# Performance work log

Measured on AMD Instinct MI355X. Metric: run time of the kernel, lower is better.

## Reference

```python
import jax, jax.numpy as jnp
import numpy as np

BUCKET_SIZE = 256
LOOK_BACKWARD = 1
LOOK_FORWARD = 0  # causal


def look_around(x, backward, forward, pad_value):
    # x: (b, n_buckets, w, ...) -> (b, n_buckets, w*(backward+forward+1), ...)
    n = x.shape[1]
    pads = [(0, 0)] * x.ndim
    pads[1] = (backward, forward)
    p = jnp.pad(x, pads, constant_values=pad_value)
    return jnp.concatenate([p[:, i:i + n] for i in range(backward + forward + 1)], axis=2)


def setup_inputs() -> dict:
    key = jax.random.key(0)
    kq, kk, kv = jax.random.split(key, 3)
    shape = (2, 16, 4096, 64)  # [batch, heads, seq, head_dim]
    q = jax.random.normal(kq, shape, dtype=jnp.float32)
    k = jax.random.normal(kk, shape, dtype=jnp.float32)
    v = jax.random.normal(kv, shape, dtype=jnp.float32)
    return {"q": q, "k": k, "v": v}


def reference(q, k, v):
    shape = q.shape
    t, e = shape[-2], shape[-1]
    merge = lambda x: x.reshape(-1, t, e)
    q, k, v = merge(q), merge(k), merge(v)
    b = q.shape[0]
    buckets = t // BUCKET_SIZE

    bucket_fn = lambda x: x.reshape(b, buckets, BUCKET_SIZE, e)
    bq, bk, bv = bucket_fn(q), bucket_fn(k), bucket_fn(v)

    bk = look_around(bk, LOOK_BACKWARD, LOOK_FORWARD, 0.0)
    bv = look_around(bv, LOOK_BACKWARD, LOOK_FORWARD, 0.0)

    ticker = jnp.arange(t, dtype=jnp.int32).reshape(1, buckets, BUCKET_SIZE)
    bq_t = ticker  # (1, buckets, w)
    bq_k = look_around(ticker, LOOK_BACKWARD, LOOK_FORWARD, -1)  # (1, buckets, w*(lb+lf+1))

    dots = jnp.einsum('bnie,bnje->bnij', bq, bk) * (e ** -0.5)
    mask_value = -jnp.finfo(dots.dtype).max

    causal_mask = bq_t[:, :, :, None] < bq_k[:, :, None, :]
    pad_mask = (bq_k == -1)[:, :, None, :]
    dots = jnp.where(causal_mask | pad_mask, mask_value, dots)

    attn = jax.nn.softmax(dots, axis=-1)
    out = jnp.einsum('bnij,bnje->bnie', attn, bv)
    return out.reshape(shape)
```

## Files before the change

### kernel.cpp

```cpp
#include <hip/hip_runtime.h>

typedef __bf16 bf16x8 __attribute__((ext_vector_type(8)));
typedef float f32x16 __attribute__((ext_vector_type(16)));
typedef int i32x2 __attribute__((ext_vector_type(2)));
typedef unsigned int u32;

#define NCH 8

static __device__ __forceinline__ u32 cvt_pk_bf16(float lo, float hi) {
    u32 r;
    asm("v_cvt_pk_bf16_f32 %0, %1, %2" : "=v"(r) : "v"(lo), "v"(hi));
    return r;
}

__global__ __launch_bounds__(512, 4)
void local_attn_kernel(const float* __restrict__ qg, const float* __restrict__ kg,
                       const float* __restrict__ vg, float* __restrict__ og)
{
    __shared__ __align__(16) __bf16 sK[2][64][64];
    __shared__ __align__(16) u32 sVp[2][64][32];

    const int bid = ((blockIdx.x & 7) << 6) | (blockIdx.x >> 3);
    const int bh = bid >> 4, bi = bid & 15;
    const int tid = threadIdx.x, w = tid >> 6;
    const int lane = tid & 63, l31 = lane & 31, h = lane >> 5;

    const long long base = (long long)bh << 18;
    const float* qp = qg + base + ((long long)bi << 14);
    const float* kp = kg + base + (((long long)(bi - 1)) << 14);
    const float* vp = vg + base + (((long long)(bi - 1)) << 14);
    float*       op = og + base + ((long long)bi << 14);

    bf16x8 qf[4];
    {
        const float QS = 0.18033688011112042f;
        const float* qrow = qp + (w * 32 + l31) * 64 + 8 * h;
#pragma unroll
        for (int ks = 0; ks < 4; ++ks) {
            float4 f0 = *(const float4*)(qrow + ks * 16);
            float4 f1 = *(const float4*)(qrow + ks * 16 + 4);
            bf16x8 t;
            t[0] = (__bf16)(f0.x * QS); t[1] = (__bf16)(f0.y * QS);
            t[2] = (__bf16)(f0.z * QS); t[3] = (__bf16)(f0.w * QS);
            t[4] = (__bf16)(f1.x * QS); t[5] = (__bf16)(f1.y * QS);
            t[6] = (__bf16)(f1.z * QS); t[7] = (__bf16)(f1.w * QS);
            qf[ks] = t;
        }
    }

    f32x16 o0, o1;
#pragma unroll
    for (int i = 0; i < 16; ++i) { o0[i] = 0.f; o1[i] = 0.f; }
    float lsum = 0.f;

    const int skey = tid >> 3, stg = tid & 7;
    const int kslot = (stg ^ (skey & 7)) << 3;
    const int vkp = tid >> 4, vd0 = (tid & 15) * 4;
    const int vkq = vkp >> 2, vj = vkp & 3;
    const float* kA = kp + skey * 64 + stg * 8;
    const float* vA = vp + (2 * vkp) * 64 + vd0;

    const int c0 = (bi == 0) ? 4 : 0;
    const int qpos = w * 32 + l31;
    const int wlim = 32 * w + 287;

    int cur = 0;
    float4 k0r, k1r, v0r, v1r;

#define STAGE_LOAD(c) do {                                   \
        const float* ks_ = kA + (c) * (64 * 64);             \
        k0r = *(const float4*)ks_;                           \
        k1r = *(const float4*)(ks_ + 4);                     \
        const float* vs_ = vA + (c) * (64 * 64);             \
        v0r = *(const float4*)vs_;                           \
        v1r = *(const float4*)(vs_ + 64);                    \
    } while (0)

#define STAGE_WRITE(buf) do {                                                     \
        union { u32 u[4]; bf16x8 b; } kv_;                                        \
        kv_.u[0] = cvt_pk_bf16(k0r.x, k0r.y);                                     \
        kv_.u[1] = cvt_pk_bf16(k0r.z, k0r.w);                                     \
        kv_.u[2] = cvt_pk_bf16(k1r.x, k1r.y);                                     \
        kv_.u[3] = cvt_pk_bf16(k1r.z, k1r.w);                                     \
        *(bf16x8*)&sK[buf][skey][kslot] = kv_.b;                                  \
        {                                                                         \
            const int r0 = vd0,     s0 = vkq ^ (r0 & 7) ^ ((r0 >> 2) & 7);        \
            const int r1 = vd0 + 1, s1 = vkq ^ (r1 & 7) ^ ((r1 >> 2) & 7);        \
            const int r2 = vd0 + 2, s2 = vkq ^ (r2 & 7) ^ ((r2 >> 2) & 7);        \
            const int r3 = vd0 + 3, s3 = vkq ^ (r3 & 7) ^ ((r3 >> 2) & 7);        \
            sVp[buf][r0][(s0 << 2) + vj] = cvt_pk_bf16(v0r.x, v1r.x);             \
            sVp[buf][r1][(s1 << 2) + vj] = cvt_pk_bf16(v0r.y, v1r.y);             \
            sVp[buf][r2][(s2 << 2) + vj] = cvt_pk_bf16(v0r.z, v1r.z);             \
            sVp[buf][r3][(s3 << 2) + vj] = cvt_pk_bf16(v0r.w, v1r.w);             \
        }                                                                         \
    } while (0)

    STAGE_LOAD(c0);
    STAGE_WRITE(0);

    for (int c = c0; c < NCH; ++c) {
        __syncthreads();
        const bool pf = (c + 1 < NCH);
        if (pf) STAGE_LOAD(c + 1);

        const int kbase = c * 64;
#pragma unroll
        for (int kt = 0; kt < 2; ++kt) {
            const int kb0 = kbase + 32 * kt;
            if (kb0 > wlim) continue;

            const int key = kt * 32 + l31;
            const int ksw = key & 7;
            bf16x8 kfa[4];
#pragma unroll
            for (int ks = 0; ks < 4; ++ks)
                kfa[ks] = *(const bf16x8*)&sK[cur][key][((ks * 2 + h) ^ ksw) << 3];
            f32x16 s;
#pragma unroll
            for (int i = 0; i < 16; ++i) s[i] = 0.f;
#pragma unroll
            for (int ks = 0; ks < 4; ++ks)
                s = __builtin_amdgcn_mfma_f32_32x32x16_bf16(kfa[ks], qf[ks], s, 0, 0, 0);

            float pv[16];
            const int jb = kb0 + 4 * h;
            if (kb0 + 31 <= 32 * w + 256) {
#pragma unroll
                for (int r = 0; r < 16; ++r) {
                    pv[r] = __builtin_amdgcn_exp2f(s[r]);
                    lsum += pv[r];
                }
            } else {
#pragma unroll
                for (int r = 0; r < 16; ++r) {
                    const int j = jb + (r & 3) + 8 * (r >> 2);
                    float e = __builtin_amdgcn_exp2f(s[r]);
                    pv[r] = (j > qpos + 256) ? 0.f : e;
                    lsum += pv[r];
                }
            }

            u32 wds[8];
#pragma unroll
            for (int m = 0; m < 8; ++m)
                wds[m] = cvt_pk_bf16(pv[2 * m], pv[2 * m + 1]);

#pragma unroll
            for (int kis = 0; kis < 2; ++kis) {
                i32x2 r02 = __builtin_amdgcn_permlane32_swap(
                    (int)wds[4 * kis + 0], (int)wds[4 * kis + 2], false, false);
                i32x2 r13 = __builtin_amdgcn_permlane32_swap(
                    (int)wds[4 * kis + 1], (int)wds[4 * kis + 3], false, false);
                union { u32 u[4]; bf16x8 b; } pu;
                pu.u[0] = (u32)r02.x; pu.u[1] = (u32)r13.x;
                pu.u[2] = (u32)r02.y; pu.u[3] = (u32)r13.y;

                const int G = (kt * 2 + kis) * 2 + h;
                const int sl = G ^ (l31 & 7) ^ ((l31 >> 2) & 7);
                bf16x8 vb0 = *(const bf16x8*)&sVp[cur][l31][sl << 2];
                bf16x8 vb1 = *(const bf16x8*)&sVp[cur][32 + l31][sl << 2];
                o0 = __builtin_amdgcn_mfma_f32_32x32x16_bf16(pu.b, vb0, o0, 0, 0, 0);
                o1 = __builtin_amdgcn_mfma_f32_32x32x16_bf16(pu.b, vb1, o1, 0, 0, 0);
            }
        }

        if (pf) STAGE_WRITE(cur ^ 1);
        cur ^= 1;
    }

    lsum += __shfl_xor(lsum, 32, 64);
    const float inv = 1.0f / lsum;
#pragma unroll
    for (int r = 0; r < 16; ++r) {
        const int qr = (r & 3) + 8 * (r >> 2) + 4 * h;
        const float iq = __shfl(inv, qr, 64);
        float* orow = op + (w * 32 + qr) * 64;
        orow[l31]      = o0[r] * iq;
        orow[32 + l31] = o1[r] * iq;
    }
}

extern "C" void kernel_launch(void* const* d_in, const int* in_sizes, int n_in,
                              void* d_out, int out_size, void* d_ws, size_t ws_size,
                              hipStream_t stream) {
    const float* q = (const float*)d_in[0];
    const float* k = (const float*)d_in[1];
    const float* v = (const float*)d_in[2];
    float* out = (float*)d_out;
    local_attn_kernel<<<dim3(512), dim3(512), 0, stream>>>(q, k, v, out);
}
```

Before: 34.15 us.

## Split each query bucket across two 256-thread blocks with causal chunk trimming

Each 256-query bucket is now handled by two blocks of 4 waves (128 queries each) instead of one block of 8 waves, doubling the grid to 1024. The first query half stops after 6 key chunks because the later chunks lie entirely beyond its causal limit, which skips K/V staging that block would never use. Each thread now stages twice as much K/V per chunk, and the keys shared by both halves are loaded and converted twice.

```diff
diff --git a/kernel.cpp b/kernel.cpp
--- a/kernel.cpp
+++ b/kernel.cpp
@@ -4,8 +4,6 @@
 typedef float f32x16 __attribute__((ext_vector_type(16)));
 typedef int i32x2 __attribute__((ext_vector_type(2)));
 typedef unsigned int u32;
-
-#define NCH 8
 
 static __device__ __forceinline__ u32 cvt_pk_bf16(float lo, float hi) {
     u32 r;
@@ -13,15 +11,15 @@
     return r;
 }
 
-__global__ __launch_bounds__(512, 4)
+__global__ __launch_bounds__(256, 4)
 void local_attn_kernel(const float* __restrict__ qg, const float* __restrict__ kg,
                        const float* __restrict__ vg, float* __restrict__ og)
 {
     __shared__ __align__(16) __bf16 sK[2][64][64];
     __shared__ __align__(16) u32 sVp[2][64][32];
 
-    const int bid = ((blockIdx.x & 7) << 6) | (blockIdx.x >> 3);
-    const int bh = bid >> 4, bi = bid & 15;
+    const int bid = ((blockIdx.x & 7) << 7) | (blockIdx.x >> 3);
+    const int bh = bid >> 5, bi = (bid >> 1) & 15, qh = bid & 1;
     const int tid = threadIdx.x, w = tid >> 6;
     const int lane = tid & 63, l31 = lane & 31, h = lane >> 5;
 
@@ -31,10 +29,12 @@
     const float* vp = vg + base + (((long long)(bi - 1)) << 14);
     float*       op = og + base + ((long long)bi << 14);
 
+    const int qb0 = qh * 128 + w * 32;
+
     bf16x8 qf[4];
     {
         const float QS = 0.18033688011112042f;
-        const float* qrow = qp + (w * 32 + l31) * 64 + 8 * h;
+        const float* qrow = qp + (qb0 + l31) * 64 + 8 * h;
 #pragma unroll
         for (int ks = 0; ks < 4; ++ks) {
             float4 f0 = *(const float4*)(qrow + ks * 16);
@@ -56,51 +56,65 @@
     const int skey = tid >> 3, stg = tid & 7;
     const int kslot = (stg ^ (skey & 7)) << 3;
     const int vkp = tid >> 4, vd0 = (tid & 15) * 4;
-    const int vkq = vkp >> 2, vj = vkp & 3;
+    const int vkq0 = vkp >> 2, vkq1 = vkq0 + 4, vj = vkp & 3;
     const float* kA = kp + skey * 64 + stg * 8;
     const float* vA = vp + (2 * vkp) * 64 + vd0;
 
     const int c0 = (bi == 0) ? 4 : 0;
-    const int qpos = w * 32 + l31;
-    const int wlim = 32 * w + 287;
+    const int NCHB = 6 + 2 * qh;
+    const int qpos = qb0 + l31;
+    const int wlim = qb0 + 287;
 
     int cur = 0;
-    float4 k0r, k1r, v0r, v1r;
+    float4 k0r, k1r, k2r, k3r, v0r, v1r, v2r, v3r;
 
 #define STAGE_LOAD(c) do {                                   \
         const float* ks_ = kA + (c) * (64 * 64);             \
         k0r = *(const float4*)ks_;                           \
         k1r = *(const float4*)(ks_ + 4);                     \
+        k2r = *(const float4*)(ks_ + 2048);                  \
+        k3r = *(const float4*)(ks_ + 2052);                  \
         const float* vs_ = vA + (c) * (64 * 64);             \
         v0r = *(const float4*)vs_;                           \
         v1r = *(const float4*)(vs_ + 64);                    \
+        v2r = *(const float4*)(vs_ + 2048);                  \
+        v3r = *(const float4*)(vs_ + 2112);                  \
     } while (0)
 
 #define STAGE_WRITE(buf) do {                                                     \
-        union { u32 u[4]; bf16x8 b; } kv_;                                        \
-        kv_.u[0] = cvt_pk_bf16(k0r.x, k0r.y);                                     \
-        kv_.u[1] = cvt_pk_bf16(k0r.z, k0r.w);                                     \
-        kv_.u[2] = cvt_pk_bf16(k1r.x, k1r.y);                                     \
-        kv_.u[3] = cvt_pk_bf16(k1r.z, k1r.w);                                     \
-        *(bf16x8*)&sK[buf][skey][kslot] = kv_.b;                                  \
+        union { u32 u[4]; bf16x8 b; } kva_, kvb_;                                 \
+        kva_.u[0] = cvt_pk_bf16(k0r.x, k0r.y);                                    \
+        kva_.u[1] = cvt_pk_bf16(k0r.z, k0r.w);                                    \
+        kva_.u[2] = cvt_pk_bf16(k1r.x, k1r.y);                                    \
+        kva_.u[3] = cvt_pk_bf16(k1r.z, k1r.w);                                    \
+        *(bf16x8*)&sK[buf][skey][kslot] = kva_.b;                                 \
+        kvb_.u[0] = cvt_pk_bf16(k2r.x, k2r.y);                                    \
+        kvb_.u[1] = cvt_pk_bf16(k2r.z, k2r.w);                                    \
+        kvb_.u[2] = cvt_pk_bf16(k3r.x, k3r.y);                                    \
+        kvb_.u[3] = cvt_pk_bf16(k3r.z, k3r.w);                                    \
+        *(bf16x8*)&sK[buf][skey + 32][kslot] = kvb_.b;                            \
         {                                                                         \
-            const int r0 = vd0,     s0 = vkq ^ (r0 & 7) ^ ((r0 >> 2) & 7);        \
-            const int r1 = vd0 + 1, s1 = vkq ^ (r1 & 7) ^ ((r1 >> 2) & 7);        \
-            const int r2 = vd0 + 2, s2 = vkq ^ (r2 & 7) ^ ((r2 >> 2) & 7);        \
-            const int r3 = vd0 + 3, s3 = vkq ^ (r3 & 7) ^ ((r3 >> 2) & 7);        \
-            sVp[buf][r0][(s0 << 2) + vj] = cvt_pk_bf16(v0r.x, v1r.x);             \
-            sVp[buf][r1][(s1 << 2) + vj] = cvt_pk_bf16(v0r.y, v1r.y);             \
-            sVp[buf][r2][(s2 << 2) + vj] = cvt_pk_bf16(v0r.z, v1r.z);             \
-            sVp[buf][r3][(s3 << 2) + vj] = cvt_pk_bf16(v0r.w, v1r.w);             \
+            const int r0 = vd0,     x0 = (r0 & 7) ^ ((r0 >> 2) & 7);              \
+            const int r1 = vd0 + 1, x1 = (r1 & 7) ^ ((r1 >> 2) & 7);              \
+            const int r2 = vd0 + 2, x2 = (r2 & 7) ^ ((r2 >> 2) & 7);              \
+            const int r3 = vd0 + 3, x3 = (r3 & 7) ^ ((r3 >> 2) & 7);              \
+            sVp[buf][r0][((vkq0 ^ x0) << 2) + vj] = cvt_pk_bf16(v0r.x, v1r.x);    \
+            sVp[buf][r1][((vkq0 ^ x1) << 2) + vj] = cvt_pk_bf16(v0r.y, v1r.y);    \
+            sVp[buf][r2][((vkq0 ^ x2) << 2) + vj] = cvt_pk_bf16(v0r.z, v1r.z);    \
+            sVp[buf][r3][((vkq0 ^ x3) << 2) + vj] = cvt_pk_bf16(v0r.w, v1r.w);    \
+            sVp[buf][r0][((vkq1 ^ x0) << 2) + vj] = cvt_pk_bf16(v2r.x, v3r.x);    \
+            sVp[buf][r1][((vkq1 ^ x1) << 2) + vj] = cvt_pk_bf16(v2r.y, v3r.y);    \
+            sVp[buf][r2][((vkq1 ^ x2) << 2) + vj] = cvt_pk_bf16(v2r.z, v3r.z);    \
+            sVp[buf][r3][((vkq1 ^ x3) << 2) + vj] = cvt_pk_bf16(v2r.w, v3r.w);    \
         }                                                                         \
     } while (0)
 
     STAGE_LOAD(c0);
     STAGE_WRITE(0);
 
-    for (int c = c0; c < NCH; ++c) {
+    for (int c = c0; c < NCHB; ++c) {
         __syncthreads();
-        const bool pf = (c + 1 < NCH);
+        const bool pf = (c + 1 < NCHB);
         if (pf) STAGE_LOAD(c + 1);
 
         const int kbase = c * 64;
@@ -124,7 +138,7 @@
 
             float pv[16];
             const int jb = kb0 + 4 * h;
-            if (kb0 + 31 <= 32 * w + 256) {
+            if (kb0 + 31 <= qb0 + 256) {
 #pragma unroll
                 for (int r = 0; r < 16; ++r) {
                     pv[r] = __builtin_amdgcn_exp2f(s[r]);
@@ -174,7 +188,7 @@
     for (int r = 0; r < 16; ++r) {
         const int qr = (r & 3) + 8 * (r >> 2) + 4 * h;
         const float iq = __shfl(inv, qr, 64);
-        float* orow = op + (w * 32 + qr) * 64;
+        float* orow = op + (qb0 + qr) * 64;
         orow[l31]      = o0[r] * iq;
         orow[32 + l31] = o1[r] * iq;
     }
@@ -187,5 +201,5 @@
     const float* k = (const float*)d_in[1];
     const float* v = (const float*)d_in[2];
     float* out = (float*)d_out;
-    local_attn_kernel<<<dim3(512), dim3(512), 0, stream>>>(q, k, v, out);
+    local_attn_kernel<<<dim3(1024), dim3(256), 0, stream>>>(q, k, v, out);
 }
```

New measurement: 53.91 us. +57.9%, slower.

## Deepen K/V register prefetch to two stages with unrolled chunk loop

Applied to the files above, without the earlier changes.

Keeps two register staging sets so the global loads of K/V chunks are issued two chunks ahead, and unrolls the chunk loop by two so each staging set has a fixed role. It also fuses the exp2 and bf16 packing into one loop, and lowers the launch-bounds occupancy hint from 4 to 2 blocks per CU to leave room for the extra registers. The aim is to hide more global-memory latency behind the MFMA work. The cost is higher register pressure and possibly lower occupancy.

```diff
diff --git a/kernel.cpp b/kernel.cpp
--- a/kernel.cpp
+++ b/kernel.cpp
@@ -5,15 +5,13 @@
 typedef int i32x2 __attribute__((ext_vector_type(2)));
 typedef unsigned int u32;
 
-#define NCH 8
-
 static __device__ __forceinline__ u32 cvt_pk_bf16(float lo, float hi) {
     u32 r;
     asm("v_cvt_pk_bf16_f32 %0, %1, %2" : "=v"(r) : "v"(lo), "v"(hi));
     return r;
 }
 
-__global__ __launch_bounds__(512, 4)
+__global__ __launch_bounds__(512, 2)
 void local_attn_kernel(const float* __restrict__ qg, const float* __restrict__ kg,
                        const float* __restrict__ vg, float* __restrict__ og)
 {
@@ -61,48 +59,39 @@
     const float* vA = vp + (2 * vkp) * 64 + vd0;
 
     const int c0 = (bi == 0) ? 4 : 0;
+    const int count = (bi == 0) ? 4 : 8;
     const int qpos = w * 32 + l31;
     const int wlim = 32 * w + 287;
 
-    int cur = 0;
-    float4 k0r, k1r, v0r, v1r;
+    struct St { float4 k0, k1, v0, v1; };
+    St stA, stB;
 
-#define STAGE_LOAD(c) do {                                   \
-        const float* ks_ = kA + (c) * (64 * 64);             \
-        k0r = *(const float4*)ks_;                           \
-        k1r = *(const float4*)(ks_ + 4);                     \
-        const float* vs_ = vA + (c) * (64 * 64);             \
-        v0r = *(const float4*)vs_;                           \
-        v1r = *(const float4*)(vs_ + 64);                    \
-    } while (0)
+    auto LD = [&](St& st, int c) {
+        const float* ks_ = kA + c * (64 * 64);
+        st.k0 = *(const float4*)ks_;
+        st.k1 = *(const float4*)(ks_ + 4);
+        const float* vs_ = vA + c * (64 * 64);
+        st.v0 = *(const float4*)vs_;
+        st.v1 = *(const float4*)(vs_ + 64);
+    };
+    auto WR = [&](const St& st, int buf) {
+        union { u32 u[4]; bf16x8 b; } kv_;
+        kv_.u[0] = cvt_pk_bf16(st.k0.x, st.k0.y);
+        kv_.u[1] = cvt_pk_bf16(st.k0.z, st.k0.w);
+        kv_.u[2] = cvt_pk_bf16(st.k1.x, st.k1.y);
+        kv_.u[3] = cvt_pk_bf16(st.k1.z, st.k1.w);
+        *(bf16x8*)&sK[buf][skey][kslot] = kv_.b;
+        const int r0 = vd0,     s0 = vkq ^ (r0 & 7) ^ ((r0 >> 2) & 7);
+        const int r1 = vd0 + 1, s1 = vkq ^ (r1 & 7) ^ ((r1 >> 2) & 7);
+        const int r2 = vd0 + 2, s2 = vkq ^ (r2 & 7) ^ ((r2 >> 2) & 7);
+        const int r3 = vd0 + 3, s3 = vkq ^ (r3 & 7) ^ ((r3 >> 2) & 7);
+        sVp[buf][r0][(s0 << 2) + vj] = cvt_pk_bf16(st.v0.x, st.v1.x);
+        sVp[buf][r1][(s1 << 2) + vj] = cvt_pk_bf16(st.v0.y, st.v1.y);
+        sVp[buf][r2][(s2 << 2) + vj] = cvt_pk_bf16(st.v0.z, st.v1.z);
+        sVp[buf][r3][(s3 << 2) + vj] = cvt_pk_bf16(st.v0.w, st.v1.w);
+    };
 
-#define STAGE_WRITE(buf) do {                                                     \
-        union { u32 u[4]; bf16x8 b; } kv_;                                        \
-        kv_.u[0] = cvt_pk_bf16(k0r.x, k0r.y);                                     \
-        kv_.u[1] = cvt_pk_bf16(k0r.z, k0r.w);                                     \
-        kv_.u[2] = cvt_pk_bf16(k1r.x, k1r.y);                                     \
-        kv_.u[3] = cvt_pk_bf16(k1r.z, k1r.w);                                     \
-        *(bf16x8*)&sK[buf][skey][kslot] = kv_.b;                                  \
-        {                                                                         \
-            const int r0 = vd0,     s0 = vkq ^ (r0 & 7) ^ ((r0 >> 2) & 7);        \
-            const int r1 = vd0 + 1, s1 = vkq ^ (r1 & 7) ^ ((r1 >> 2) & 7);        \
-            const int r2 = vd0 + 2, s2 = vkq ^ (r2 & 7) ^ ((r2 >> 2) & 7);        \
-            const int r3 = vd0 + 3, s3 = vkq ^ (r3 & 7) ^ ((r3 >> 2) & 7);        \
-            sVp[buf][r0][(s0 << 2) + vj] = cvt_pk_bf16(v0r.x, v1r.x);             \
-            sVp[buf][r1][(s1 << 2) + vj] = cvt_pk_bf16(v0r.y, v1r.y);             \
-            sVp[buf][r2][(s2 << 2) + vj] = cvt_pk_bf16(v0r.z, v1r.z);             \
-            sVp[buf][r3][(s3 << 2) + vj] = cvt_pk_bf16(v0r.w, v1r.w);             \
-        }                                                                         \
-    } while (0)
-
-    STAGE_LOAD(c0);
-    STAGE_WRITE(0);
-
-    for (int c = c0; c < NCH; ++c) {
-        __syncthreads();
-        const bool pf = (c + 1 < NCH);
-        if (pf) STAGE_LOAD(c + 1);
-
+    auto COMPUTE = [&](int c, int cur) {
         const int kbase = c * 64;
 #pragma unroll
         for (int kt = 0; kt < 2; ++kt) {
@@ -117,33 +106,35 @@
                 kfa[ks] = *(const bf16x8*)&sK[cur][key][((ks * 2 + h) ^ ksw) << 3];
             f32x16 s;
 #pragma unroll
-            for (int i = 0; i < 16; ++i) s[i] = 0.f;
+            for (int i2 = 0; i2 < 16; ++i2) s[i2] = 0.f;
 #pragma unroll
             for (int ks = 0; ks < 4; ++ks)
                 s = __builtin_amdgcn_mfma_f32_32x32x16_bf16(kfa[ks], qf[ks], s, 0, 0, 0);
 
-            float pv[16];
-            const int jb = kb0 + 4 * h;
+            u32 wds[8];
             if (kb0 + 31 <= 32 * w + 256) {
 #pragma unroll
-                for (int r = 0; r < 16; ++r) {
-                    pv[r] = __builtin_amdgcn_exp2f(s[r]);
-                    lsum += pv[r];
+                for (int m = 0; m < 8; ++m) {
+                    const float e0 = __builtin_amdgcn_exp2f(s[2 * m]);
+                    const float e1 = __builtin_amdgcn_exp2f(s[2 * m + 1]);
+                    lsum += e0 + e1;
+                    wds[m] = cvt_pk_bf16(e0, e1);
                 }
             } else {
+                const int jb = kb0 + 4 * h;
 #pragma unroll
-                for (int r = 0; r < 16; ++r) {
-                    const int j = jb + (r & 3) + 8 * (r >> 2);
-                    float e = __builtin_amdgcn_exp2f(s[r]);
-                    pv[r] = (j > qpos + 256) ? 0.f : e;
-                    lsum += pv[r];
+                for (int m = 0; m < 8; ++m) {
+                    const int r0 = 2 * m, r1 = 2 * m + 1;
+                    const int j0 = jb + (r0 & 3) + 8 * (r0 >> 2);
+                    const int j1 = jb + (r1 & 3) + 8 * (r1 >> 2);
+                    float e0 = __builtin_amdgcn_exp2f(s[r0]);
+                    float e1 = __builtin_amdgcn_exp2f(s[r1]);
+                    e0 = (j0 > qpos + 256) ? 0.f : e0;
+                    e1 = (j1 > qpos + 256) ? 0.f : e1;
+                    lsum += e0 + e1;
+                    wds[m] = cvt_pk_bf16(e0, e1);
                 }
             }
-
-            u32 wds[8];
-#pragma unroll
-            for (int m = 0; m < 8; ++m)
-                wds[m] = cvt_pk_bf16(pv[2 * m], pv[2 * m + 1]);
 
 #pragma unroll
             for (int kis = 0; kis < 2; ++kis) {
@@ -163,8 +154,24 @@
                 o1 = __builtin_amdgcn_mfma_f32_32x32x16_bf16(pu.b, vb1, o1, 0, 0, 0);
             }
         }
+    };
 
-        if (pf) STAGE_WRITE(cur ^ 1);
+    LD(stA, c0);
+    LD(stB, c0 + 1);
+    WR(stA, 0);
+    int cur = 0;
+
+    for (int i = 0; i < count; i += 2) {
+        __syncthreads();
+        if (i + 2 < count) LD(stA, c0 + i + 2);
+        COMPUTE(c0 + i, cur);
+        WR(stB, cur ^ 1);
+        cur ^= 1;
+
+        __syncthreads();
+        if (i + 3 < count) LD(stB, c0 + i + 3);
+        COMPUTE(c0 + i + 1, cur);
+        if (i + 2 < count) WR(stA, cur ^ 1);
         cur ^= 1;
     }
 
```

Result: slower. 39.90 us (+16.8%).
